# Kernel tuning notes

Hardware: AMD Instinct MI355X
Metric: run time of the kernel (lower is better)

Reference implementation:

```python
import jax, jax.numpy as jnp
import numpy as np

K = 64          # type_num = len(unique(rna_label)); static for jit
TAU = 0.5       # args.info_nce_tau
EPS = 1e-8


def _prototypes(feat, label):
    # per-class mean over the N axis: feat [N,D], label [N] in [0,K)
    s = jax.ops.segment_sum(feat, label, num_segments=K)               # [K,D]
    c = jax.ops.segment_sum(jnp.ones(feat.shape[0], feat.dtype), label, num_segments=K)
    return s / c[:, None]


def _l2norm(x):
    # torch F.normalize(dim=1): x / max(||x||, 1e-12)
    n = jnp.sqrt(jnp.sum(x * x, axis=1, keepdims=True))
    return x / jnp.maximum(n, 1e-12)


def setup_inputs() -> dict:
    key = jax.random.key(0)
    k1, k2, k3, k4 = jax.random.split(key, 4)
    N, D = 100000, 256
    return {
        "atac_feature": jax.random.normal(k1, (N, D), dtype=jnp.float32),
        "rna_feature": jax.random.normal(k2, (N, D), dtype=jnp.float32),
        "atac_label": jax.random.randint(k3, (N,), 0, K, dtype=jnp.int32),
        "rna_label": jax.random.randint(k4, (N,), 0, K, dtype=jnp.int32),
    }


def reference(atac_feature, rna_feature, atac_label, rna_label):
    A = _l2norm(_prototypes(atac_feature, atac_label))   # [K,D]
    R = _l2norm(_prototypes(rna_feature, rna_label))     # [K,D]

    # Fp[k] = exp(A[k] * R[k] / tau), elementwise over D
    Fp = jnp.exp(A * R / TAU)                             # [K,D]

    # pairwise elementwise-product exps: [K,K,D]
    Sa = jnp.exp(A[:, None, :] * A[None, :, :] / TAU)
    Sr = jnp.exp(A[:, None, :] * R[None, :, :] / TAU)

    off = (1.0 - jnp.eye(K, dtype=A.dtype))[:, :, None]   # exclude j == k
    # Fn[k] = sum_{j!=k}(Sa[k,j] + Fp[k]) + sum_{j!=k}(Sr[k,j] + Fp[k])
    Fn = ((Sa + Sr) * off).sum(axis=1) + 2.0 * (K - 1) * Fp

    loss_k = (-jnp.log(Fp / (Fn + EPS))).mean(axis=1)     # [K]
    return loss_k.sum()
```

## Files before the change

### kernel.cpp

```cpp
#include <hip/hip_runtime.h>
#include <math.h>

#define KK 64
#define DD 256
#define GX 256
#define TROWS 32
#define MAXCHUNK 512
#define INV_TAU 2.0f
#define EPSL 1e-8f

typedef __attribute__((address_space(1))) const void gvoid;
typedef __attribute__((address_space(3))) void svoid;


__global__ __launch_bounds__(256) void seg_partial_kernel(
    const float* __restrict__ fa, const float* __restrict__ fr,
    const int* __restrict__ la, const int* __restrict__ lr,
    float* __restrict__ P, float* __restrict__ C, int N)
{
    __shared__ float stage[2][TROWS * DD];
    __shared__ int lbl[MAXCHUNK];
    __shared__ int cnt[KK];

    const int tid = threadIdx.x;
    const int g = blockIdx.x, f = blockIdx.y;
    const float* __restrict__ feat = f ? fr : fa;
    const int* __restrict__ label = f ? lr : la;

    if (tid < KK) cnt[tid] = 0;

    const int chunk = (N + GX - 1) / GX;
    const int n0 = g * chunk;
    int rows = min(N, n0 + chunk) - n0;
    if (rows < 0) rows = 0;

    __syncthreads();
    for (int i = tid; i < rows; i += 256) lbl[i] = label[n0 + i];
    __syncthreads();
    for (int i = tid; i < rows; i += 256) atomicAdd(&cnt[lbl[i]], 1);

    float accr[KK];
    #pragma unroll
    for (int k = 0; k < KK; ++k) accr[k] = 0.0f;

    const int nt = (rows + TROWS - 1) / TROWS;
    const int w = tid >> 6, lane = tid & 63;
    const size_t limit = (size_t)N * DD - 4;

    #define STAGE(t)                                                                     \
    do {                                                                                 \
        const size_t base_ = ((size_t)(n0 + (t) * TROWS)) * DD + (size_t)w * 2048 + lane * 4; \
        float* lb_ = &stage[(t) & 1][w * 2048];                                          \
        _Pragma("unroll")                                                                \
        for (int i_ = 0; i_ < 8; ++i_) {                                                 \
            size_t e_ = base_ + i_ * 256;                                                \
            if (e_ > limit) e_ = 0;                    \
            __builtin_amdgcn_global_load_lds((gvoid*)(feat + e_), (svoid*)(lb_ + i_ * 256), 16, 0, 0); \
        }                                                                                \
    } while (0)

    if (nt > 0) STAGE(0);
    for (int t = 0; t < nt; ++t) {
        if (t + 1 < nt) {
            STAGE(t + 1);
            asm volatile("s_waitcnt vmcnt(8)" ::: "memory");
        } else {
            asm volatile("s_waitcnt vmcnt(0)" ::: "memory");
        }
        __builtin_amdgcn_s_barrier();

        const int rn = min(TROWS, rows - t * TROWS);
        const float* sb = stage[t & 1];
        const int* lb = lbl + t * TROWS;
        const int myl = (lane < rn) ? lb[lane] : -1;

        #pragma unroll
        for (int k = 0; k < KK; ++k) {
            unsigned long long m = __ballot(myl == k);
            while (m) {
                const int r = (int)__builtin_ctzll(m);
                m &= m - 1;
                accr[k] += sb[r * DD + tid];
            }
        }

        asm volatile("s_waitcnt lgkmcnt(0)" ::: "memory");
        __builtin_amdgcn_s_barrier();
    }

    float* dst = P + ((size_t)f * GX + g) * (KK * DD) + tid;
    #pragma unroll
    for (int k = 0; k < KK; ++k) dst[(size_t)k * DD] = accr[k];
    __syncthreads();
    if (tid < KK) C[((size_t)f * GX + g) * KK + tid] = (float)cnt[tid];
    #undef STAGE
}

__global__ __launch_bounds__(256) void proto_norm_kernel(
    const float* __restrict__ P, const float* __restrict__ C,
    float* __restrict__ AR, int G)
{
    const int k = blockIdx.x, f = blockIdx.y, tid = threadIdx.x;
    const float* base = P + (size_t)f * G * (KK * DD) + (size_t)k * DD + tid;

    float s = 0.0f;
    int g = 0;
    for (; g + 8 <= G; g += 8) {
        float v[8];
        #pragma unroll
        for (int u = 0; u < 8; ++u) v[u] = base[(size_t)(g + u) * (KK * DD)];
        #pragma unroll
        for (int u = 0; u < 8; ++u) s += v[u];
    }
    for (; g < G; ++g) s += base[(size_t)g * (KK * DD)];

    float c = 0.0f;
    const float* cb = C + (size_t)f * G * KK + k;
    for (int g2 = 0; g2 < G; ++g2) c += cb[(size_t)g2 * KK];

    const float m = s / c;
    float sq = m * m;
    #pragma unroll
    for (int i = 1; i < 64; i <<= 1) sq += __shfl_xor(sq, i, 64);
    __shared__ float red[4];
    const int wid = tid >> 6, lane = tid & 63;
    if (lane == 0) red[wid] = sq;
    __syncthreads();
    const float nrm = red[0] + red[1] + red[2] + red[3];
    AR[(size_t)f * KK * DD + (size_t)k * DD + tid] = m / fmaxf(sqrtf(nrm), 1e-12f);
}

__global__ __launch_bounds__(256) void loss_kernel(const float* __restrict__ AR,
                                                   float* __restrict__ lossk)
{
    const float* A = AR;
    const float* R = AR + KK * DD;
    const int k = blockIdx.x, tid = threadIdx.x;

    const float a = A[k * DD + tid];
    const float r = R[k * DD + tid];
    const float lfp = a * r * INV_TAU;
    const float fp = expf(lfp);
    float ssa = 0.0f, ssr = 0.0f;
    #pragma unroll 8
    for (int j = 0; j < KK; ++j) {
        ssa += expf(a * A[j * DD + tid] * INV_TAU);
        ssr += expf(a * R[j * DD + tid] * INV_TAU);
    }
    const float Fn = (ssa - expf(a * a * INV_TAU)) + (ssr - fp) + 2.0f * (KK - 1) * fp;
    float l = logf(Fn + EPSL) - lfp;

    #pragma unroll
    for (int i = 1; i < 64; i <<= 1) l += __shfl_xor(l, i, 64);
    __shared__ float red[4];
    const int wid = tid >> 6, lane = tid & 63;
    if (lane == 0) red[wid] = l;
    __syncthreads();
    if (tid == 0) lossk[k] = (red[0] + red[1] + red[2] + red[3]) * (1.0f / DD);
}

__global__ void final_kernel(const float* __restrict__ lossk, float* __restrict__ out)
{
    float v = lossk[threadIdx.x];
    #pragma unroll
    for (int i = 1; i < 64; i <<= 1) v += __shfl_xor(v, i, 64);
    if (threadIdx.x == 0) out[0] = v;
}

extern "C" void kernel_launch(void* const* d_in, const int* in_sizes, int n_in,
                              void* d_out, int out_size, void* d_ws, size_t ws_size,
                              hipStream_t stream)
{
    const float* fa = (const float*)d_in[0];
    const float* fr = (const float*)d_in[1];
    const int* la = (const int*)d_in[2];
    const int* lr = (const int*)d_in[3];
    float* ws = (float*)d_ws;
    float* out = (float*)d_out;
    const int N = in_sizes[2];

    float* P = ws;
    float* C = P + 2L * GX * KK * DD;
    float* AR = C + 2L * GX * KK;
    float* lossk = AR + 2L * KK * DD;

    seg_partial_kernel<<<dim3(GX, 2), 256, 0, stream>>>(fa, fr, la, lr, P, C, N);
    proto_norm_kernel<<<dim3(KK, 2), 256, 0, stream>>>(P, C, AR, GX);
    loss_kernel<<<KK, 256, 0, stream>>>(AR, lossk);
    final_kernel<<<1, 64, 0, stream>>>(lossk, out);
}
```

Measured before the change: 123.9 us.

## Give each wave private LDS staging and split rows across two wave groups

Reworks the segment-sum kernel to use 512 threads, with each wave owning a 64-column slice and its own double-buffered LDS staging area. Two wave groups take alternating 16-row tiles, and their partial sums are merged through LDS at the end. This drops the block-wide barriers per tile and lets waves stream independently, with more waves per block to hide memory latency. In exchange it uses 4-byte global_load_lds loads instead of 16-byte ones, issuing more load instructions, and adds a final LDS reduction step.

```diff
diff --git a/kernel.cpp b/kernel.cpp
--- a/kernel.cpp
+++ b/kernel.cpp
@@ -4,7 +4,7 @@
 #define KK 64
 #define DD 256
 #define GX 256
-#define TROWS 32
+#define MT 16
 #define MAXCHUNK 512
 #define INV_TAU 2.0f
 #define EPSL 1e-8f
@@ -13,12 +13,12 @@
 typedef __attribute__((address_space(3))) void svoid;
 
 
-__global__ __launch_bounds__(256) void seg_partial_kernel(
+__global__ __launch_bounds__(512, 4) void seg_partial_kernel(
     const float* __restrict__ fa, const float* __restrict__ fr,
     const int* __restrict__ la, const int* __restrict__ lr,
     float* __restrict__ P, float* __restrict__ C, int N)
 {
-    __shared__ float stage[2][TROWS * DD];
+    __shared__ __attribute__((aligned(16))) float stg[8][2][MT * 64];
     __shared__ int lbl[MAXCHUNK];
     __shared__ int cnt[KK];
 
@@ -35,44 +35,49 @@
     if (rows < 0) rows = 0;
 
     __syncthreads();
-    for (int i = tid; i < rows; i += 256) lbl[i] = label[n0 + i];
-    __syncthreads();
-    for (int i = tid; i < rows; i += 256) atomicAdd(&cnt[lbl[i]], 1);
+    for (int i = tid; i < rows; i += 512) lbl[i] = label[n0 + i];
+    __syncthreads();
+    for (int i = tid; i < rows; i += 512) atomicAdd(&cnt[lbl[i]], 1);
+
+    const int w = tid >> 6, lane = tid & 63;
+    const int q = w & 3;
+    const int s = w >> 2;
+    const int col0 = q * 64;
 
     float accr[KK];
     #pragma unroll
     for (int k = 0; k < KK; ++k) accr[k] = 0.0f;
 
-    const int nt = (rows + TROWS - 1) / TROWS;
-    const int w = tid >> 6, lane = tid & 63;
-    const size_t limit = (size_t)N * DD - 4;
-
-    #define STAGE(t)                                                                     \
-    do {                                                                                 \
-        const size_t base_ = ((size_t)(n0 + (t) * TROWS)) * DD + (size_t)w * 2048 + lane * 4; \
-        float* lb_ = &stage[(t) & 1][w * 2048];                                          \
-        _Pragma("unroll")                                                                \
-        for (int i_ = 0; i_ < 8; ++i_) {                                                 \
-            size_t e_ = base_ + i_ * 256;                                                \
-            if (e_ > limit) e_ = 0;                    \
-            __builtin_amdgcn_global_load_lds((gvoid*)(feat + e_), (svoid*)(lb_ + i_ * 256), 16, 0, 0); \
-        }                                                                                \
+    #define STAGEW(j, b)                                                        \
+    do {                                                                        \
+        const int base_ = (j) * MT;                                             \
+        float* lb_ = &stg[w][b][0];                                             \
+        _Pragma("unroll")                                                       \
+        for (int i_ = 0; i_ < MT; ++i_) {                                       \
+            const int row_ = n0 + base_ + i_;                                   \
+            size_t e_ = (size_t)row_ * DD + col0 + lane;                        \
+            if (row_ >= N) e_ = 0;                       \
+            __builtin_amdgcn_global_load_lds((gvoid*)(feat + e_),               \
+                                             (svoid*)(lb_ + i_ * 64), 4, 0, 0);\
+        }                                                                       \
     } while (0)
 
-    if (nt > 0) STAGE(0);
-    for (int t = 0; t < nt; ++t) {
-        if (t + 1 < nt) {
-            STAGE(t + 1);
-            asm volatile("s_waitcnt vmcnt(8)" ::: "memory");
+    const int nmt = (rows + MT - 1) / MT;
+    int pb = 0;
+    if (s < nmt) STAGEW(s, 0);
+    for (int j = s; j < nmt; j += 2) {
+        const int jn = j + 2;
+        if (jn < nmt) {
+            STAGEW(jn, pb ^ 1);
+            asm volatile("s_waitcnt vmcnt(16)" ::: "memory");
         } else {
             asm volatile("s_waitcnt vmcnt(0)" ::: "memory");
         }
-        __builtin_amdgcn_s_barrier();
-
-        const int rn = min(TROWS, rows - t * TROWS);
-        const float* sb = stage[t & 1];
-        const int* lb = lbl + t * TROWS;
-        const int myl = (lane < rn) ? lb[lane] : -1;
+
+        const int base = j * MT;
+        const int idx = base + lane;
+        const int myl = (lane < MT && idx < rows) ? lbl[idx] : -1;
+        const float* sb = &stg[w][pb][0];
 
         #pragma unroll
         for (int k = 0; k < KK; ++k) {
@@ -80,20 +85,29 @@
             while (m) {
                 const int r = (int)__builtin_ctzll(m);
                 m &= m - 1;
-                accr[k] += sb[r * DD + tid];
+                accr[k] += sb[r * 64 + lane];
             }
         }
-
-        asm volatile("s_waitcnt lgkmcnt(0)" ::: "memory");
-        __builtin_amdgcn_s_barrier();
-    }
-
-    float* dst = P + ((size_t)f * GX + g) * (KK * DD) + tid;
-    #pragma unroll
-    for (int k = 0; k < KK; ++k) dst[(size_t)k * DD] = accr[k];
-    __syncthreads();
+        pb ^= 1;
+    }
+    #undef STAGEW
+
+    __syncthreads();
+    float* sf = (float*)stg;
+    if (s == 1) {
+        #pragma unroll
+        for (int k = 0; k < KK; ++k) sf[q * 4096 + k * 64 + lane] = accr[k];
+    }
+    __syncthreads();
+    if (s == 0) {
+        float* dstb = P + ((size_t)f * GX + g) * (KK * DD);
+        #pragma unroll
+        for (int k = 0; k < KK; ++k) {
+            const float v = accr[k] + sf[q * 4096 + k * 64 + lane];
+            dstb[(size_t)k * DD + col0 + lane] = v;
+        }
+    }
     if (tid < KK) C[((size_t)f * GX + g) * KK + tid] = (float)cnt[tid];
-    #undef STAGE
 }
 
 __global__ __launch_bounds__(256) void proto_norm_kernel(
@@ -184,7 +198,7 @@
     float* AR = C + 2L * GX * KK;
     float* lossk = AR + 2L * KK * DD;
 
-    seg_partial_kernel<<<dim3(GX, 2), 256, 0, stream>>>(fa, fr, la, lr, P, C, N);
+    seg_partial_kernel<<<dim3(GX, 2), 512, 0, stream>>>(fa, fr, la, lr, P, C, N);
     proto_norm_kernel<<<dim3(KK, 2), 256, 0, stream>>>(P, C, AR, GX);
     loss_kernel<<<KK, 256, 0, stream>>>(AR, lossk);
     final_kernel<<<1, 64, 0, stream>>>(lossk, out);
```

After: 125.0 us. No clear change (+0.8%).
